# Kernel tuning notes

Hardware: AMD Instinct MI355X
Metric: run time of the kernel (lower is better)

## Reference

```python
import jax, jax.numpy as jnp
import numpy as np

B, N, DIM, H = 2, 2048, 1024, 16
HD = DIM // H
SCALE = HD ** -0.5


def setup_inputs() -> dict:
    key = jax.random.key(0)
    ks = jax.random.split(key, 11)
    std = DIM ** -0.5
    inp = {
        'q': jax.random.normal(ks[0], (B, N, DIM), jnp.float32),
        'k': jax.random.normal(ks[1], (B, N, DIM), jnp.float32),
        'v': jax.random.normal(ks[2], (B, N, DIM), jnp.float32),
        # causal mask, broadcast over batch and heads; mask==0 -> masked out
        'mask': jnp.tril(jnp.ones((N, N), jnp.int32))[None, None],
        'Wq': jax.random.normal(ks[3], (DIM, DIM), jnp.float32) * std,
        'bq': jnp.zeros((DIM,), jnp.float32),
        'Wk': jax.random.normal(ks[4], (DIM, DIM), jnp.float32) * std,
        'bk': jnp.zeros((DIM,), jnp.float32),
        'Wv': jax.random.normal(ks[5], (DIM, DIM), jnp.float32) * std,
        'bv': jnp.zeros((DIM,), jnp.float32),
        'Wo': jax.random.normal(ks[6], (DIM, DIM), jnp.float32) * std,
        'bo': jnp.zeros((DIM,), jnp.float32),
    }
    return inp


def _split_heads(x):  # [b, n, dim] -> [b, h, n, c]
    b, n, _ = x.shape
    return x.reshape(b, n, H, HD).transpose(0, 2, 1, 3)


def reference(q, k, v, mask, Wq, bq, Wk, bk, Wv, bv, Wo, bo):
    qh = _split_heads(q @ Wq.T + bq)                      # [b,h,nq,c]
    kh = _split_heads(k @ Wk.T + bk)                      # [b,h,nk,c]
    vh = _split_heads(v @ Wv.T + bv)                      # [b,h,nk,c]
    attn = jnp.einsum('bhqc,bhkc->bhqk', qh, kh) * SCALE  # [b,h,nq,nk]
    attn = jnp.where(mask == 0, -jnp.inf, attn)
    attn = jax.nn.softmax(attn, axis=-1)
    out = jnp.einsum('bhqk,bhkc->bhqc', attn, vh)          # [b,h,nq,c]
    b, h, n, c = out.shape
    out = out.transpose(0, 2, 1, 3).reshape(b, n, h * c)   # [b,nq,dim]
    return out @ Wo.T + bo
```

## Files before the change

kernel.cpp:

```cpp
#include <hip/hip_runtime.h>

#define NN 2048
#define DIMD 1024
#define HH 16
#define HDD 64
#define SC2 0.1803368801111244f

typedef __attribute__((ext_vector_type(8))) short bf16x8;
typedef __attribute__((ext_vector_type(4))) float f32x4;
typedef __attribute__((ext_vector_type(4))) _Float16 f16x4;
typedef unsigned short ushort_t;
typedef unsigned int uint_t;

#define MFMA32(a, b, c) __builtin_amdgcn_mfma_f32_16x16x32_bf16((a), (b), (c), 0, 0, 0)
#define MFMA16H(a, b, c) __builtin_amdgcn_mfma_f32_16x16x16f16((a), (b), (c), 0, 0, 0)

__device__ __forceinline__ ushort_t f2bf(float f) {
    union { float f; uint_t u; } v; v.f = f;
    uint_t u = v.u;
    return (ushort_t)((u + 0x7FFFu + ((u >> 16) & 1u)) >> 16);
}
__device__ __forceinline__ void gl_lds16(const ushort_t* g, ushort_t* l) {
    __builtin_amdgcn_global_load_lds(
        (const __attribute__((address_space(1))) void*)g,
        (__attribute__((address_space(3))) void*)l, 16, 0, 0);
}

__global__ __launch_bounds__(256) void convert_k(
    const float* __restrict__ q, const float* __restrict__ k, const float* __restrict__ v,
    const float* __restrict__ wq, const float* __restrict__ wk,
    const float* __restrict__ wv, const float* __restrict__ wo,
    ushort_t* __restrict__ Abf, ushort_t* __restrict__ Wbf) {
    size_t gid = (size_t)blockIdx.x * 256 + threadIdx.x;
    size_t e = gid * 8;
    const float* src; ushort_t* dst;
    float sc = 1.f;
    if (e < 12582912) {
        int i = (int)(e >> 22);
        src = (i == 0 ? q : (i == 1 ? k : v)) + (e & 4194303);
        dst = Abf + e;
    } else {
        size_t e2 = e - 12582912;
        int i = (int)(e2 >> 20);
        src = (i == 0 ? wq : (i == 1 ? wk : (i == 2 ? wv : wo))) + (e2 & 1048575);
        dst = Wbf + e2;
        if (i == 0) sc = SC2;
    }
    float4 x = ((const float4*)src)[0], y = ((const float4*)src)[1];
    union { uint4 u; ushort_t s[8]; } pk;
    pk.s[0] = f2bf(x.x * sc); pk.s[1] = f2bf(x.y * sc); pk.s[2] = f2bf(x.z * sc); pk.s[3] = f2bf(x.w * sc);
    pk.s[4] = f2bf(y.x * sc); pk.s[5] = f2bf(y.y * sc); pk.s[6] = f2bf(y.z * sc); pk.s[7] = f2bf(y.w * sc);
    *(uint4*)dst = pk.u;
}

template<int MODE, int TM>
__global__ __launch_bounds__(256, TM == 128 ? 3 : 5) void gemm_k(
    const ushort_t* __restrict__ Abase, const ushort_t* __restrict__ Wbase,
    const float* __restrict__ b0p, const float* __restrict__ b1p, const float* __restrict__ b2p,
    ushort_t* __restrict__ d0, ushort_t* __restrict__ d1, ushort_t* __restrict__ d2,
    float* __restrict__ fout) {
    const int K = 1024;
    constexpr int MT = TM / 32;
    __shared__ ushort_t As[2][TM * 32];
    __shared__ ushort_t Bs[2][128 * 32];
    int z = (MODE == 0) ? blockIdx.z : 0;
    const ushort_t* A = Abase + (size_t)z * 4096 * 1024;
    const ushort_t* W = Wbase + (size_t)z * 1024 * 1024;
    const float* bias = (MODE == 0) ? (z == 0 ? b0p : (z == 1 ? b1p : b2p)) : b0p;
    int tid = threadIdx.x;
    int m0 = blockIdx.x * TM, n0 = blockIdx.y * 128;
    int lane = tid & 63, wave = tid >> 6;
    int quad = lane >> 4, l15 = lane & 15;
    int wm = (wave >> 1) * (TM / 2), wn = (wave & 1) * 64;

    f32x4 acc[MT][4];
    for (int i = 0; i < MT; i++)
        for (int j = 0; j < 4; j++)
            acc[i][j] = (f32x4){0.f, 0.f, 0.f, 0.f};

    int rA = tid >> 2, cA = tid & 3;
    int gA = cA ^ ((rA >> 1) & 3);

    auto stage = [&](int buf, int k0) {
        gl_lds16(A + (size_t)(m0 + rA) * K + k0 + gA * 8, &As[buf][tid * 8]);
        if (TM == 128)
            gl_lds16(A + (size_t)(m0 + rA + 64) * K + k0 + gA * 8, &As[buf][(tid + 256) * 8]);
        gl_lds16(W + (size_t)(n0 + rA) * K + k0 + gA * 8, &Bs[buf][tid * 8]);
        gl_lds16(W + (size_t)(n0 + rA + 64) * K + k0 + gA * 8, &Bs[buf][(tid + 256) * 8]);
    };
    stage(0, 0);

    int fc = (quad ^ ((l15 >> 1) & 3)) * 8;

    for (int it = 0; it < 32; it++) {
        int cur = it & 1;
        __syncthreads();
        if (it < 31) stage(1 - cur, (it + 1) * 32);
        bf16x8 a[MT], b[4];
        for (int mt = 0; mt < MT; mt++)
            a[mt] = *(const bf16x8*)&As[cur][(wm + mt * 16 + l15) * 32 + fc];
        for (int nt = 0; nt < 4; nt++)
            b[nt] = *(const bf16x8*)&Bs[cur][(wn + nt * 16 + l15) * 32 + fc];
        for (int mt = 0; mt < MT; mt++)
            for (int nt = 0; nt < 4; nt++)
                acc[mt][nt] = MFMA32(a[mt], b[nt], acc[mt][nt]);
    }
    if (MODE == 0 && z == 2) {
        for (int nt = 0; nt < 4; nt++) {
            int n = n0 + wn + nt * 16 + l15;
            float bv = bias[n];
            int h = n >> 6, c = n & 63;
            for (int mt = 0; mt < MT; mt++) {
                int mb = m0 + wm + mt * 16 + quad * 4;
                int b = mb >> 11, ns = mb & 2047;
                union { uint2 u2; _Float16 hh[4]; } pkv;
                pkv.hh[0] = (_Float16)(acc[mt][nt][0] + bv);
                pkv.hh[1] = (_Float16)(acc[mt][nt][1] + bv);
                pkv.hh[2] = (_Float16)(acc[mt][nt][2] + bv);
                pkv.hh[3] = (_Float16)(acc[mt][nt][3] + bv);
                *(uint2*)&d2[(((size_t)(b * HH + h)) * HDD + c) * NN + ns] = pkv.u2;
            }
        }
    } else {
        for (int nt = 0; nt < 4; nt++) {
            int n = n0 + wn + nt * 16 + l15;
            float bv = bias[n];
            if (MODE == 0 && z == 0) bv *= SC2;
            for (int mt = 0; mt < MT; mt++)
                for (int r = 0; r < 4; r++) {
                    int m = m0 + wm + mt * 16 + quad * 4 + r;
                    float val = acc[mt][nt][r] + bv;
                    if (MODE == 0) {
                        int b = m >> 11, ns = m & 2047;
                        int h = n >> 6, c = n & 63;
                        ushort_t* dst = (z == 0) ? d0 : d1;
                        dst[(((size_t)(b * HH + h)) * NN + ns) * HDD + c] = f2bf(val);
                    } else {
                        fout[(size_t)m * DIMD + n] = val;
                    }
                }
        }
    }
}

__global__ __launch_bounds__(256, 3) void attn7(const ushort_t* __restrict__ Qh,
                                                const ushort_t* __restrict__ Kh,
                                                const ushort_t* __restrict__ VtG,
                                                ushort_t* __restrict__ aout) {
    __shared__ ushort_t Kb[3][64 * 64];
    __shared__ ushort_t Vb[3][64 * 64];
    int tid = threadIdx.x, lane = tid & 63, w = tid >> 6;
    int quad = lane >> 4, l15 = lane & 15;
    int bh = blockIdx.y;
    int p = blockIdx.x;
    int tile = (w & 2) ? (63 - p) : p;
    int ka = tile >> 1;
    int kc = (63 - p) >> 1;
    int rowb = tile * 32 + (w & 1) * 16;
    const ushort_t* Qp = Qh + (size_t)bh * NN * HDD;
    const ushort_t* Kp = Kh + (size_t)bh * NN * HDD;
    const ushort_t* Vp = VtG + (size_t)bh * HDD * NN;

    bf16x8 aq[2];
    for (int kk = 0; kk < 2; kk++)
        aq[kk] = *(const bf16x8*)&Qp[(size_t)(rowb + l15) * HDD + kk * 32 + quad * 8];

    f32x4 o[4];
    for (int ct = 0; ct < 4; ct++)
        o[ct] = (f32x4){0.f, 0.f, 0.f, 0.f};
    float l = 0.f;

    int sr0 = tid >> 3, scg = tid & 7;
    int sr1 = sr0 + 32;
    int ssc = scg ^ (sr0 & 7);
    int key = l15 & 7;
    int c0 = (quad ^ key) * 8;
    int c1 = ((4 + quad) ^ key) * 8;

    auto stageK = [&](int s, int kt) {
        gl_lds16(Kp + (size_t)(kt * 64 + sr0) * 64 + ssc * 8, &Kb[s][(0 * 256 + w * 64) * 8]);
        gl_lds16(Kp + (size_t)(kt * 64 + sr1) * 64 + ssc * 8, &Kb[s][(1 * 256 + w * 64) * 8]);
        gl_lds16(Vp + (size_t)sr0 * NN + kt * 64 + ssc * 8, &Vb[s][(0 * 256 + w * 64) * 8]);
        gl_lds16(Vp + (size_t)sr1 * NN + kt * 64 + ssc * 8, &Vb[s][(1 * 256 + w * 64) * 8]);
    };
    stageK(0, 0);
    stageK(1, 1);

    int cur = 0;
    for (int kb = 0; kb <= kc; kb++) {
        if (kb < kc)
            asm volatile("s_waitcnt vmcnt(4)\ns_barrier" ::: "memory");
        else
            asm volatile("s_waitcnt vmcnt(0)\ns_barrier" ::: "memory");
        if (kb + 2 <= kc) stageK(cur == 0 ? 2 : cur - 1, kb + 2);
        if (kb <= ka) {
            bf16x8 kf0[4], kf1[4];
            for (int nt = 0; nt < 4; nt++) {
                kf0[nt] = *(const bf16x8*)&Kb[cur][(nt * 16 + l15) * 64 + c0];
                kf1[nt] = *(const bf16x8*)&Kb[cur][(nt * 16 + l15) * 64 + c1];
            }
            f16x4 vf[4][4];
            for (int ct = 0; ct < 4; ct++)
                for (int nt = 0; nt < 4; nt++)
                    vf[ct][nt] = *(const f16x4*)&Vb[cur][(ct * 16 + l15) * 64 +
                                    ((2 * nt + (quad >> 1)) ^ key) * 8 + (quad & 1) * 4];
            f32x4 s[4];
            __builtin_amdgcn_s_setprio(1);
            for (int nt = 0; nt < 4; nt++) {
                f32x4 z = (f32x4){0.f, 0.f, 0.f, 0.f};
                z = MFMA32(kf0[nt], aq[0], z);
                s[nt] = MFMA32(kf1[nt], aq[1], z);
            }
            __builtin_amdgcn_s_setprio(0);
            f16x4 ap[4];
            if (kb == ka) {
                for (int nt = 0; nt < 4; nt++)
                    for (int r = 0; r < 4; r++) {
                        int kv = kb * 64 + nt * 16 + quad * 4 + r;
                        float pp = (kv <= rowb + l15) ? exp2f(s[nt][r]) : 0.f;
                        ap[nt][r] = (_Float16)pp; l += pp;
                    }
            } else {
                for (int nt = 0; nt < 4; nt++)
                    for (int r = 0; r < 4; r++) {
                        float pp = exp2f(s[nt][r]);
                        ap[nt][r] = (_Float16)pp; l += pp;
                    }
            }
            __builtin_amdgcn_s_setprio(1);
            for (int ct = 0; ct < 4; ct++)
                for (int nt = 0; nt < 4; nt++)
                    o[ct] = MFMA16H(ap[nt], vf[ct][nt], o[ct]);
            __builtin_amdgcn_s_setprio(0);
        }
        cur = (cur == 2) ? 0 : cur + 1;
    }

    l += __shfl_xor(l, 16); l += __shfl_xor(l, 32);

    int b = bh >> 4, h = bh & 15;
    for (int r = 0; r < 4; r++) {
        float il = 1.f / __shfl(l, quad * 4 + r);
        for (int ct = 0; ct < 4; ct++) {
            int c = ct * 16 + l15;
            int qq = rowb + quad * 4 + r;
            aout[((size_t)(b * NN + qq)) * DIMD + h * HDD + c] = f2bf(o[ct][r] * il);
        }
    }
}

extern "C" void kernel_launch(void* const* d_in, const int* in_sizes, int n_in,
                              void* d_out, int out_size, void* d_ws, size_t ws_size,
                              hipStream_t stream) {
    const float* q  = (const float*)d_in[0];
    const float* k  = (const float*)d_in[1];
    const float* v  = (const float*)d_in[2];
    const float* Wq = (const float*)d_in[4];
    const float* bq = (const float*)d_in[5];
    const float* Wk = (const float*)d_in[6];
    const float* bk = (const float*)d_in[7];
    const float* Wv = (const float*)d_in[8];
    const float* bv = (const float*)d_in[9];
    const float* Wo = (const float*)d_in[10];
    const float* bo = (const float*)d_in[11];
    float* out = (float*)d_out;

    char* ws = (char*)d_ws;
    ushort_t* Abf  = (ushort_t*)(ws);
    ushort_t* Wbf  = (ushort_t*)(ws + (24ull << 20));
    ushort_t* Qh   = (ushort_t*)(ws + (32ull << 20));
    ushort_t* Kh   = (ushort_t*)(ws + (40ull << 20));
    ushort_t* VtG  = (ushort_t*)(ws + (48ull << 20));
    ushort_t* AObf = (ushort_t*)(ws + (56ull << 20));

    hipLaunchKernelGGL(convert_k, dim3(8192), dim3(256), 0, stream,
                       q, k, v, Wq, Wk, Wv, Wo, Abf, Wbf);
    hipLaunchKernelGGL((gemm_k<0, 128>), dim3(32, 8, 3), dim3(256), 0, stream,
                       Abf, Wbf, bq, bk, bv, Qh, Kh, VtG, (float*)nullptr);
    hipLaunchKernelGGL(attn7, dim3(32, 32), dim3(256), 0, stream, Qh, Kh, VtG, AObf);
    hipLaunchKernelGGL((gemm_k<1, 64>), dim3(64, 8, 1), dim3(256), 0, stream,
                       AObf, Wbf + 3ull * 1024 * 1024, bo, nullptr, nullptr,
                       nullptr, nullptr, nullptr, out);
}
```

Measured before the change: 259.3 us.

## Pair mirrored query tiles per block sharing 128-key double-buffered K/V stages

```diff
diff --git a/kernel.cpp b/kernel.cpp
--- a/kernel.cpp
+++ b/kernel.cpp
@@ -9,6 +9,7 @@
 typedef __attribute__((ext_vector_type(8))) short bf16x8;
 typedef __attribute__((ext_vector_type(4))) float f32x4;
 typedef __attribute__((ext_vector_type(4))) _Float16 f16x4;
+typedef __attribute__((ext_vector_type(2))) __fp16 hf16x2;
 typedef unsigned short ushort_t;
 typedef unsigned int uint_t;
 
@@ -143,108 +144,139 @@
     }
 }
 
-__global__ __launch_bounds__(256, 3) void attn7(const ushort_t* __restrict__ Qh,
+__global__ __launch_bounds__(256, 2) void attn9(const ushort_t* __restrict__ Qh,
                                                 const ushort_t* __restrict__ Kh,
                                                 const ushort_t* __restrict__ VtG,
                                                 ushort_t* __restrict__ aout) {
-    __shared__ ushort_t Kb[3][64 * 64];
-    __shared__ ushort_t Vb[3][64 * 64];
+    __shared__ ushort_t Kb[2][2][64 * 64];
+    __shared__ ushort_t Vb[2][2][64 * 64];
     int tid = threadIdx.x, lane = tid & 63, w = tid >> 6;
     int quad = lane >> 4, l15 = lane & 15;
     int bh = blockIdx.y;
-    int p = blockIdx.x;
-    int tile = (w & 2) ? (63 - p) : p;
-    int ka = tile >> 1;
-    int kc = (63 - p) >> 1;
-    int rowb = tile * 32 + (w & 1) * 16;
+    int qa = blockIdx.x;
+    int qc = 31 - qa;
     const ushort_t* Qp = Qh + (size_t)bh * NN * HDD;
     const ushort_t* Kp = Kh + (size_t)bh * NN * HDD;
     const ushort_t* Vp = VtG + (size_t)bh * HDD * NN;
-
-    bf16x8 aq[2];
-    for (int kk = 0; kk < 2; kk++)
-        aq[kk] = *(const bf16x8*)&Qp[(size_t)(rowb + l15) * HDD + kk * 32 + quad * 8];
-
-    f32x4 o[4];
-    for (int ct = 0; ct < 4; ct++)
-        o[ct] = (f32x4){0.f, 0.f, 0.f, 0.f};
-    float l = 0.f;
+    int ra = qa * 64 + w * 16;
+    int rc = qc * 64 + w * 16;
+
+    bf16x8 aqa[2], aqc[2];
+    for (int kk = 0; kk < 2; kk++) {
+        aqa[kk] = *(const bf16x8*)&Qp[(size_t)(ra + l15) * HDD + kk * 32 + quad * 8];
+        aqc[kk] = *(const bf16x8*)&Qp[(size_t)(rc + l15) * HDD + kk * 32 + quad * 8];
+    }
+    asm volatile("" :: "v"(aqa[0]), "v"(aqa[1]), "v"(aqc[0]), "v"(aqc[1]));
+
+    f32x4 oa[4], oc[4], ola, olc;
+    for (int ct = 0; ct < 4; ct++) {
+        oa[ct] = (f32x4){0.f, 0.f, 0.f, 0.f};
+        oc[ct] = (f32x4){0.f, 0.f, 0.f, 0.f};
+    }
+    ola = (f32x4){0.f, 0.f, 0.f, 0.f};
+    olc = (f32x4){0.f, 0.f, 0.f, 0.f};
+    const f16x4 vone = {(_Float16)1.f, (_Float16)1.f, (_Float16)1.f, (_Float16)1.f};
 
     int sr0 = tid >> 3, scg = tid & 7;
-    int sr1 = sr0 + 32;
     int ssc = scg ^ (sr0 & 7);
     int key = l15 & 7;
     int c0 = (quad ^ key) * 8;
     int c1 = ((4 + quad) ^ key) * 8;
 
     auto stageK = [&](int s, int kt) {
-        gl_lds16(Kp + (size_t)(kt * 64 + sr0) * 64 + ssc * 8, &Kb[s][(0 * 256 + w * 64) * 8]);
-        gl_lds16(Kp + (size_t)(kt * 64 + sr1) * 64 + ssc * 8, &Kb[s][(1 * 256 + w * 64) * 8]);
-        gl_lds16(Vp + (size_t)sr0 * NN + kt * 64 + ssc * 8, &Vb[s][(0 * 256 + w * 64) * 8]);
-        gl_lds16(Vp + (size_t)sr1 * NN + kt * 64 + ssc * 8, &Vb[s][(1 * 256 + w * 64) * 8]);
+        for (int h = 0; h < 2; h++) {
+            int kr = kt * 128 + h * 64;
+            gl_lds16(Kp + (size_t)(kr + sr0) * HDD + ssc * 8,      &Kb[s][h][(0 * 256 + w * 64) * 8]);
+            gl_lds16(Kp + (size_t)(kr + sr0 + 32) * HDD + ssc * 8, &Kb[s][h][(1 * 256 + w * 64) * 8]);
+            gl_lds16(Vp + (size_t)sr0 * NN + kr + ssc * 8,         &Vb[s][h][(0 * 256 + w * 64) * 8]);
+            gl_lds16(Vp + (size_t)(sr0 + 32) * NN + kr + ssc * 8,  &Vb[s][h][(1 * 256 + w * 64) * 8]);
+        }
     };
+
+    int kbmax = qc >> 1;
+    int kam   = qa >> 1;
     stageK(0, 0);
-    stageK(1, 1);
+
+    auto doHalf = [&](const bf16x8 (&aq)[2], f32x4 (&o)[4], f32x4& ol,
+                      int rowb, const ushort_t* Kl, const ushort_t* Vl,
+                      int kvb, bool diag) {
+        bf16x8 kf0[4], kf1[4];
+        for (int nt = 0; nt < 4; nt++) {
+            kf0[nt] = *(const bf16x8*)&Kl[(nt * 16 + l15) * 64 + c0];
+            kf1[nt] = *(const bf16x8*)&Kl[(nt * 16 + l15) * 64 + c1];
+        }
+        f32x4 s[4];
+        __builtin_amdgcn_s_setprio(1);
+        for (int nt = 0; nt < 4; nt++) {
+            f32x4 z = (f32x4){0.f, 0.f, 0.f, 0.f};
+            z = MFMA32(kf0[nt], aq[0], z);
+            s[nt] = MFMA32(kf1[nt], aq[1], z);
+        }
+        __builtin_amdgcn_s_setprio(0);
+        f16x4 ap[4];
+        if (diag) {
+            for (int nt = 0; nt < 4; nt++) {
+                float pp[4];
+                for (int r = 0; r < 4; r++) {
+                    int kv = kvb + nt * 16 + quad * 4 + r;
+                    pp[r] = (kv <= rowb + l15) ? __builtin_amdgcn_exp2f(s[nt][r]) : 0.f;
+                }
+                union { hf16x2 h2[2]; f16x4 h4; } u;
+                u.h2[0] = __builtin_amdgcn_cvt_pkrtz(pp[0], pp[1]);
+                u.h2[1] = __builtin_amdgcn_cvt_pkrtz(pp[2], pp[3]);
+                ap[nt] = u.h4;
+            }
+        } else {
+            for (int nt = 0; nt < 4; nt++) {
+                union { hf16x2 h2[2]; f16x4 h4; } u;
+                u.h2[0] = __builtin_amdgcn_cvt_pkrtz(__builtin_amdgcn_exp2f(s[nt][0]),
+                                                     __builtin_amdgcn_exp2f(s[nt][1]));
+                u.h2[1] = __builtin_amdgcn_cvt_pkrtz(__builtin_amdgcn_exp2f(s[nt][2]),
+                                                     __builtin_amdgcn_exp2f(s[nt][3]));
+                ap[nt] = u.h4;
+            }
+        }
+        f16x4 vf[4][4];
+        for (int ct = 0; ct < 4; ct++)
+            for (int nt = 0; nt < 4; nt++)
+                vf[ct][nt] = *(const f16x4*)&Vl[(ct * 16 + l15) * 64 +
+                                ((2 * nt + (quad >> 1)) ^ key) * 8 + (quad & 1) * 4];
+        __builtin_amdgcn_s_setprio(1);
+        for (int nt = 0; nt < 4; nt++)
+            ol = MFMA16H(ap[nt], vone, ol);
+        for (int ct = 0; ct < 4; ct++)
+            for (int nt = 0; nt < 4; nt++)
+                o[ct] = MFMA16H(ap[nt], vf[ct][nt], o[ct]);
+        __builtin_amdgcn_s_setprio(0);
+    };
 
     int cur = 0;
-    for (int kb = 0; kb <= kc; kb++) {
-        if (kb < kc)
-            asm volatile("s_waitcnt vmcnt(4)\ns_barrier" ::: "memory");
-        else
-            asm volatile("s_waitcnt vmcnt(0)\ns_barrier" ::: "memory");
-        if (kb + 2 <= kc) stageK(cur == 0 ? 2 : cur - 1, kb + 2);
-        if (kb <= ka) {
-            bf16x8 kf0[4], kf1[4];
-            for (int nt = 0; nt < 4; nt++) {
-                kf0[nt] = *(const bf16x8*)&Kb[cur][(nt * 16 + l15) * 64 + c0];
-                kf1[nt] = *(const bf16x8*)&Kb[cur][(nt * 16 + l15) * 64 + c1];
-            }
-            f16x4 vf[4][4];
-            for (int ct = 0; ct < 4; ct++)
-                for (int nt = 0; nt < 4; nt++)
-                    vf[ct][nt] = *(const f16x4*)&Vb[cur][(ct * 16 + l15) * 64 +
-                                    ((2 * nt + (quad >> 1)) ^ key) * 8 + (quad & 1) * 4];
-            f32x4 s[4];
-            __builtin_amdgcn_s_setprio(1);
-            for (int nt = 0; nt < 4; nt++) {
-                f32x4 z = (f32x4){0.f, 0.f, 0.f, 0.f};
-                z = MFMA32(kf0[nt], aq[0], z);
-                s[nt] = MFMA32(kf1[nt], aq[1], z);
-            }
-            __builtin_amdgcn_s_setprio(0);
-            f16x4 ap[4];
-            if (kb == ka) {
-                for (int nt = 0; nt < 4; nt++)
-                    for (int r = 0; r < 4; r++) {
-                        int kv = kb * 64 + nt * 16 + quad * 4 + r;
-                        float pp = (kv <= rowb + l15) ? exp2f(s[nt][r]) : 0.f;
-                        ap[nt][r] = (_Float16)pp; l += pp;
-                    }
-            } else {
-                for (int nt = 0; nt < 4; nt++)
-                    for (int r = 0; r < 4; r++) {
-                        float pp = exp2f(s[nt][r]);
-                        ap[nt][r] = (_Float16)pp; l += pp;
-                    }
-            }
-            __builtin_amdgcn_s_setprio(1);
-            for (int ct = 0; ct < 4; ct++)
-                for (int nt = 0; nt < 4; nt++)
-                    o[ct] = MFMA16H(ap[nt], vf[ct][nt], o[ct]);
-            __builtin_amdgcn_s_setprio(0);
-        }
-        cur = (cur == 2) ? 0 : cur + 1;
-    }
-
-    l += __shfl_xor(l, 16); l += __shfl_xor(l, 32);
+    for (int kb2 = 0; kb2 <= kbmax; kb2++) {
+        __syncthreads();
+        if (kb2 < kbmax) stageK(cur ^ 1, kb2 + 1);
+        bool dc = (kb2 == kbmax);
+        for (int h = 0; h < 2; h++)
+            doHalf(aqc, oc, olc, rc, &Kb[cur][h][0], &Vb[cur][h][0],
+                   kb2 * 128 + h * 64, dc);
+        if (kb2 <= kam) {
+            bool da = (kb2 == kam);
+            for (int h = 0; h < 2; h++)
+                doHalf(aqa, oa, ola, ra, &Kb[cur][h][0], &Vb[cur][h][0],
+                       kb2 * 128 + h * 64, da);
+        }
+        cur ^= 1;
+    }
 
     int b = bh >> 4, h = bh & 15;
     for (int r = 0; r < 4; r++) {
-        float il = 1.f / __shfl(l, quad * 4 + r);
+        float ila = 1.f / ola[r];
+        float ilc = 1.f / olc[r];
         for (int ct = 0; ct < 4; ct++) {
             int c = ct * 16 + l15;
-            int qq = rowb + quad * 4 + r;
-            aout[((size_t)(b * NN + qq)) * DIMD + h * HDD + c] = f2bf(o[ct][r] * il);
+            int qqa = ra + quad * 4 + r;
+            int qqc = rc + quad * 4 + r;
+            aout[((size_t)(b * NN + qqa)) * DIMD + h * HDD + c] = f2bf(oa[ct][r] * ila);
+            aout[((size_t)(b * NN + qqc)) * DIMD + h * HDD + c] = f2bf(oc[ct][r] * ilc);
         }
     }
 }
@@ -277,7 +309,7 @@
                        q, k, v, Wq, Wk, Wv, Wo, Abf, Wbf);
     hipLaunchKernelGGL((gemm_k<0, 128>), dim3(32, 8, 3), dim3(256), 0, stream,
                        Abf, Wbf, bq, bk, bv, Qh, Kh, VtG, (float*)nullptr);
-    hipLaunchKernelGGL(attn7, dim3(32, 32), dim3(256), 0, stream, Qh, Kh, VtG, AObf);
+    hipLaunchKernelGGL(attn9, dim3(16, 32), dim3(256), 0, stream, Qh, Kh, VtG, AObf);
     hipLaunchKernelGGL((gemm_k<1, 64>), dim3(64, 8, 1), dim3(256), 0, stream,
                        AObf, Wbf + 3ull * 1024 * 1024, bo, nullptr, nullptr,
                        nullptr, nullptr, nullptr, out);
```

Result: faster. 221.0 us, median of 3 (-14.8%).
